# Kernel tuning notes

Measured on AMD Instinct MI355X. Metric: run time of the kernel, lower is better.

## Reference

```python
import jax, jax.numpy as jnp
import numpy as np
from jax import lax

B_, NCH, T = 128, 22, 1000
F1, F2 = 8, 16
BN_EPS = 1e-5


def _conv(x, w, b, pad, groups=1):
    y = lax.conv_general_dilated(x, w, (1, 1), pad,
                                 dimension_numbers=('NCHW', 'OIHW', 'NCHW'),
                                 feature_group_count=groups)
    return y if b is None else y + b[None, :, None, None]


def _bn(x, g, b):
    # eval-mode BatchNorm2d with running_mean=0, running_var=1
    return x * (g / np.sqrt(1.0 + BN_EPS))[None, :, None, None] + b[None, :, None, None]


def _avgpool(x, w, s):
    y = lax.reduce_window(x, 0.0, lax.add, (1, 1, 1, w), (1, 1, 1, s), 'VALID')
    return y / w


def _ln(x, g, b):
    m = x.mean(-1, keepdims=True)
    v = ((x - m) ** 2).mean(-1, keepdims=True)
    return (x - m) * lax.rsqrt(v + 1e-5) * g + b


def _enc_layer(h, qw, qb, pw, pb, f1w, f1b, f2w, f2b, g1, b1, g2, b2):
    # h: (S, N, E). Torch TransformerEncoderLayer default is seq-first, so axis 0
    # (the STDCNN batch dim) is attended over -- faithfully reproduced here.
    S, N, E = h.shape
    H = 8
    hd = E // H
    q, k, v = jnp.split(h @ qw.T + qb, 3, axis=-1)
    q = q.reshape(S, N, H, hd)
    k = k.reshape(S, N, H, hd)
    v = v.reshape(S, N, H, hd)
    att = jax.nn.softmax(jnp.einsum('snhd,tnhd->nhst', q, k) / np.sqrt(hd), axis=-1)
    o = jnp.einsum('nhst,tnhd->snhd', att, v).reshape(S, N, E) @ pw.T + pb
    h = _ln(h + o, g1, b1)
    ff = jax.nn.relu(h @ f1w.T + f1b) @ f2w.T + f2b
    return _ln(h + ff, g2, b2)


def setup_inputs() -> dict:
    key = jax.random.key(0)
    ks = iter(jax.random.split(key, 48))

    def nrm(shape, s=0.1):
        return jax.random.normal(next(ks), shape, jnp.float32) * s

    inp = dict(
        x=jax.random.normal(next(ks), (B_, 1, NCH, T), jnp.float32),
        w_spec1=nrm((F1, 1, 1, 125)), b_spec1=nrm((F1,)),
        w_spec2=nrm((F1, 1, 1, 30)), b_spec2=nrm((F1,)),
        g_bn1=1.0 + nrm((F1,)), b_bn1=nrm((F1,)),
        g_bn2=1.0 + nrm((F1,)), b_bn2=nrm((F1,)),
        w_sp1a=nrm((F2, 1, NCH, 1)),
        g_bn3=1.0 + nrm((F2,)), b_bn3=nrm((F2,)),
        w_sp1b=nrm((F2, F2, 1, 1)), b_sp1b=nrm((F2,)),
        g_bn4=1.0 + nrm((F2,)), b_bn4=nrm((F2,)),
        w_sp2=nrm((F2, F1, NCH, 1)), b_sp2=nrm((F2,)),
        g_bn5=1.0 + nrm((F2,)), b_bn5=nrm((F2,)),
        A=jnp.eye(F2, dtype=jnp.float32) + nrm((F2, F2), 0.01),
        Bm=nrm((F2, F2)),
        Cm=jnp.eye(F2, dtype=jnp.float32) + nrm((F2, F2), 0.01),
        qkv_w=nrm((2, 3 * F2, F2)), qkv_b=nrm((2, 3 * F2)),
        proj_w=nrm((2, F2, F2)), proj_b=nrm((2, F2)),
        ff1_w=nrm((2, 64, F2)), ff1_b=nrm((2, 64)),
        ff2_w=nrm((2, F2, 64)), ff2_b=nrm((2, F2)),
        ln1_g=jnp.ones((2, F2), jnp.float32), ln1_b=jnp.zeros((2, F2), jnp.float32),
        ln2_g=jnp.ones((2, F2), jnp.float32), ln2_b=jnp.zeros((2, F2), jnp.float32),
    )
    return inp


def reference(x, w_spec1, b_spec1, w_spec2, b_spec2, g_bn1, b_bn1, g_bn2, b_bn2,
              w_sp1a, g_bn3, b_bn3, w_sp1b, b_sp1b, g_bn4, b_bn4,
              w_sp2, b_sp2, g_bn5, b_bn5, A, Bm, Cm,
              qkv_w, qkv_b, proj_w, proj_b, ff1_w, ff1_b, ff2_w, ff2_b,
              ln1_g, ln1_b, ln2_g, ln2_b):
    # spectral branches (torch 'same' padding: k=125 -> (62,62); k=30 -> (14,15))
    x1 = _bn(_conv(x, w_spec1, b_spec1, [(0, 0), (62, 62)]), g_bn1, b_bn1)
    x2 = _bn(_conv(x, w_spec2, b_spec2, [(0, 0), (14, 15)]), g_bn2, b_bn2)
    # spatial branch 1 (dropout is identity in eval)
    s1 = jax.nn.elu(_bn(_conv(x1, w_sp1a, None, 'VALID', groups=F1), g_bn3, b_bn3))
    s1 = jax.nn.elu(_bn(_conv(s1, w_sp1b, b_sp1b, 'VALID'), g_bn4, b_bn4))
    s1 = _avgpool(s1, 32, 32)                                   # (B,16,1,31)
    # spatial branch 2: square -> avgpool -> log(clamp)
    s2 = _bn(_conv(x2, w_sp2, b_sp2, 'VALID'), g_bn5, b_bn5)
    s2 = jnp.log(jnp.clip(_avgpool(jnp.square(s2), 75, 25), 1e-6))  # (B,16,1,38)
    xc = jnp.concatenate([s1, s2], axis=3)                       # (B,16,1,69)
    Bn, Cc, H2, W2 = xc.shape
    seq = xc.reshape(Bn, Cc, H2 * W2).transpose(0, 2, 1)         # (B,L,16)

    # linear SSM recurrence (torch for-loop -> lax.scan)
    def step(state, xt):
        state = state @ A + xt @ Bm.T
        return state, state @ Cm.T

    _, outs = lax.scan(step, jnp.zeros((Bn, F2), seq.dtype), seq.transpose(1, 0, 2))
    h = outs.transpose(1, 0, 2)                                  # (B,L,16)

    for l in range(2):
        h = _enc_layer(h, qkv_w[l], qkv_b[l], proj_w[l], proj_b[l],
                       ff1_w[l], ff1_b[l], ff2_w[l], ff2_b[l],
                       ln1_g[l], ln1_b[l], ln2_g[l], ln2_b[l])

    return h.reshape(Bn, W2, 1, Cc).transpose(0, 3, 2, 1)        # (B,16,1,69)
```

## Files before the change

kernel.cpp:

```cpp
#include <hip/hip_runtime.h>
#include <hip/hip_bf16.h>
#include <math.h>

#define BBATCH 128
#define NCHAN  22
#define TLEN   1000
#define F1C    8
#define F2C    16
#define L1W    31
#define L2W    38
#define LSEQ   69
#define EDIM   16
#define NHEAD  8
#define FFDIM  64

#define C_SA   0
#define C_BA   16
#define C_BC2  32
#define C_W1P  3120
#define C_AW   (C_W1P + 1024)
#define C_TOTAL (C_AW + 5632)

#define OFF_CONST 0
#define OFF_CHNK  16384
#define OFF_SEQ   (OFF_CHNK + 81920)
#define OFF_STB   (OFF_SEQ + 141312)
#define OFF_HBUF  (OFF_STB + 141312)

typedef __attribute__((ext_vector_type(8))) short bf16x8;
typedef __attribute__((ext_vector_type(4))) float f32x4;

static __device__ __forceinline__ unsigned short f2bf(float f) {
    unsigned u = __float_as_uint(f);
    unsigned r = (u + 0x7FFFu + ((u >> 16) & 1u)) >> 16;
    return (unsigned short)r;
}

#define SWZ(v, imm) __int_as_float(__builtin_amdgcn_ds_swizzle(__float_as_int(v), imm))
#define MV16(dst, sv, W) do { \
    float p0=SWZ(sv,0x010)*W[0],  p1=SWZ(sv,0x030)*W[1],  \
          p2=SWZ(sv,0x050)*W[2],  p3=SWZ(sv,0x070)*W[3],  \
          p4=SWZ(sv,0x090)*W[4],  p5=SWZ(sv,0x0B0)*W[5],  \
          p6=SWZ(sv,0x0D0)*W[6],  p7=SWZ(sv,0x0F0)*W[7],  \
          p8=SWZ(sv,0x110)*W[8],  p9=SWZ(sv,0x130)*W[9],  \
          p10=SWZ(sv,0x150)*W[10],p11=SWZ(sv,0x170)*W[11],\
          p12=SWZ(sv,0x190)*W[12],p13=SWZ(sv,0x1B0)*W[13],\
          p14=SWZ(sv,0x1D0)*W[14],p15=SWZ(sv,0x1F0)*W[15];\
    dst = (((p0+p1)+(p2+p3))+((p4+p5)+(p6+p7))) + (((p8+p9)+(p10+p11))+((p12+p13)+(p14+p15))); \
} while(0)

__global__ void k_setup(const float* __restrict__ wsp1a, const float* __restrict__ b_spec1,
                        const float* __restrict__ g_bn1, const float* __restrict__ b_bn1,
                        const float* __restrict__ g_bn3, const float* __restrict__ b_bn3,
                        const float* __restrict__ w_spec2, const float* __restrict__ b_spec2,
                        const float* __restrict__ g_bn2, const float* __restrict__ b_bn2,
                        const float* __restrict__ w_sp2, const float* __restrict__ b_sp2,
                        const float* __restrict__ g_bn5, const float* __restrict__ b_bn5,
                        const float* __restrict__ w_spec1,
                        float* __restrict__ consts)
{
    int tid = threadIdx.x;
    int gb = blockIdx.x;
    int NG = gridDim.x;
    int gid = gb*256 + tid;
    float rbn = rsqrtf(1.0f + 1e-5f);
    if (gb == 0 && tid < 16) {
        int c2 = tid, c1 = c2 >> 1;
        float wsum = 0.f;
        for (int h = 0; h < NCHAN; h++) wsum += wsp1a[c2*NCHAN + h];
        float s1b = g_bn1[c1] * rbn;
        float s3  = g_bn3[c2] * rbn;
        float C1  = (s1b * b_spec1[c1] + b_bn1[c1]) * wsum;
        consts[C_SA + c2] = s3 * s1b;
        consts[C_BA + c2] = s3 * C1 + b_bn3[c2];
        float s5 = g_bn5[c2] * rbn;
        float acc = b_sp2[c2];
        for (int cc = 0; cc < F1C; cc++) {
            float s2b = g_bn2[cc] * rbn;
            float cb  = s2b * b_spec2[cc] + b_bn2[cc];
            float wsh = 0.f;
            for (int h = 0; h < NCHAN; h++) wsh += w_sp2[(c2*F1C + cc)*NCHAN + h];
            acc += wsh * cb;
        }
        consts[C_BC2 + c2] = s5 * acc + b_bn5[c2];
    }
    for (int idx = gid; idx < 8*128; idx += 256*NG) {
        int c1 = idx >> 7, k = idx & 127;
        consts[C_W1P + idx] = (k < 125) ? w_spec1[c1*125 + k] : 0.f;
    }
    unsigned* aw = (unsigned*)&consts[C_AW];
    for (int idx = gid; idx < 22*64*4; idx += 256*NG) {
        int r = idx & 3;
        int l = (idx >> 2) & 63;
        int c = idx >> 8;
        int m = l & 15;
        int k0 = ((l >> 4) << 3) + 2*r;
        float s5 = g_bn5[m] * rbn;
        float w0 = 0.f, w1 = 0.f;
        for (int cc = 0; cc < F1C; cc++) {
            float f = w_sp2[(m*F1C + cc)*NCHAN + c] * (g_bn2[cc] * rbn);
            if (k0 < 30)     w0 += f * w_spec2[cc*30 + k0];
            if (k0 + 1 < 30) w1 += f * w_spec2[cc*30 + k0 + 1];
        }
        w0 *= s5; w1 *= s5;
        aw[idx] = (unsigned)f2bf(w0) | ((unsigned)f2bf(w1) << 16);
    }
}

#define P1 260
#define P2 132
#define PW 132
#define PB2 288
#define SQP2 257
#define FRONT_SM 10448

__device__ __forceinline__ void b1f_body(float* smem, int bid,
    const float* __restrict__ x, const float* __restrict__ wsp1a,
    const float* __restrict__ consts,
    const float* __restrict__ w_sp1b, const float* __restrict__ b_sp1b,
    const float* __restrict__ g_bn4, const float* __restrict__ b_bn4,
    float* __restrict__ seq)
{
    float* mrow = smem;
    float* econv = smem + 16*P1;
    float* wlds = smem + 16*P1 + 16*P2;
    int q = bid & 7, b = bid >> 3;
    int tid = threadIdx.x;
    int t0 = q * 128;
    int NT = (q == 7) ? 104 : 128;
    int NCOL = NT + 124;

    for (int j = tid; j < NCOL; j += 256) {
        int t = t0 - 62 + j;
        float xv[NCHAN];
#pragma unroll
        for (int h = 0; h < NCHAN; h++)
            xv[h] = ((unsigned)t < 1000u) ? x[(b*NCHAN + h)*TLEN + t] : 0.f;
#pragma unroll
        for (int c2 = 0; c2 < 16; c2++) {
            float s = 0.f;
#pragma unroll
            for (int h = 0; h < NCHAN; h++) s += wsp1a[c2*NCHAN + h] * xv[h];
            mrow[c2*P1 + j] = s;
        }
    }
    for (int j = NCOL + tid; j < P1; j += 256) {
#pragma unroll
        for (int c2 = 0; c2 < 16; c2++) mrow[c2*P1 + j] = 0.f;
    }
    for (int i = tid; i < 1024; i += 256)
        wlds[(i >> 7)*PW + (i & 127)] = consts[C_W1P + i];
    __syncthreads();

    {
        int c2 = tid & 15, seg = tid >> 4, c1 = c2 >> 1;
        if (seg < ((NT + 7) >> 3)) {
            int u0 = seg * 8;
            const float* mr = &mrow[c2*P1 + u0];
            float sa = consts[C_SA + c2], ba = consts[C_BA + c2];
            float v[12];
            {
                float4 a0 = *(const float4*)&mr[0];
                float4 a1 = *(const float4*)&mr[4];
                float4 a2 = *(const float4*)&mr[8];
                v[0]=a0.x; v[1]=a0.y; v[2]=a0.z; v[3]=a0.w;
                v[4]=a1.x; v[5]=a1.y; v[6]=a1.z; v[7]=a1.w;
                v[8]=a2.x; v[9]=a2.y; v[10]=a2.z; v[11]=a2.w;
            }
            float acc[8];
#pragma unroll
            for (int u = 0; u < 8; u++) acc[u] = 0.f;
#pragma unroll
            for (int k0 = 0; k0 < 128; k0 += 4) {
                float w0 = wlds[c1*PW + k0 + 0];
                float w1 = wlds[c1*PW + k0 + 1];
                float w2 = wlds[c1*PW + k0 + 2];
                float w3 = wlds[c1*PW + k0 + 3];
#pragma unroll
                for (int u = 0; u < 8; u++) {
                    acc[u] += w0 * v[u+0];
                    acc[u] += w1 * v[u+1];
                    acc[u] += w2 * v[u+2];
                    acc[u] += w3 * v[u+3];
                }
                if (k0 < 124) {
#pragma unroll
                    for (int i = 0; i < 8; i++) v[i] = v[i+4];
                    float4 nv = *(const float4*)&mr[k0 + 12];
                    v[8]=nv.x; v[9]=nv.y; v[10]=nv.z; v[11]=nv.w;
                }
            }
            float e[8];
#pragma unroll
            for (int u = 0; u < 8; u++) {
                float a = sa * acc[u] + ba;
                e[u] = (a > 0.f) ? a : (expf(a) - 1.f);
            }
            float* ec = &econv[c2*P2 + u0];
            *(float4*)&ec[0] = make_float4(e[0], e[1], e[2], e[3]);
            *(float4*)&ec[4] = make_float4(e[4], e[5], e[6], e[7]);
        }
    }
    __syncthreads();

    if (tid < 128) {
        int u = tid;
        int w = 4*q + (u >> 5);
        float rbn = rsqrtf(1.0f + 1e-5f);
        float hv[16];
#pragma unroll
        for (int c = 0; c < 16; c++) hv[c] = econv[c*P2 + u];
        float p[16];
#pragma unroll
        for (int c = 0; c < 16; c++) {
            float s = 0.f;
#pragma unroll
            for (int j = 0; j < 16; j++) s += w_sp1b[c*16 + j] * hv[j];
            float sc = g_bn4[c] * rbn;
            float a = sc * (s + b_sp1b[c]) + b_bn4[c];
            float g = (a > 0.f) ? a : (expf(a) - 1.f);
            g += __shfl_xor(g, 1, 64);
            g += __shfl_xor(g, 2, 64);
            g += __shfl_xor(g, 4, 64);
            g += __shfl_xor(g, 8, 64);
            g += __shfl_xor(g, 16, 64);
            p[c] = g;
        }
        if ((u & 31) == 0 && w < L1W) {
            float* sp = &seq[(b*LSEQ + w)*16];
#pragma unroll
            for (int i = 0; i < 4; i++)
                *(float4*)&sp[4*i] = make_float4(p[4*i]*(1.f/32.f), p[4*i+1]*(1.f/32.f),
                                                 p[4*i+2]*(1.f/32.f), p[4*i+3]*(1.f/32.f));
        }
    }
}

__device__ __forceinline__ void b2mm_body(float* smem, int bid,
    const float* __restrict__ x, const float* __restrict__ consts,
    float* __restrict__ chnk)
{
    unsigned short* xs = (unsigned short*)smem;
    float* sq = smem + 6336;
    const unsigned* __restrict__ awg = (const unsigned*)&consts[C_AW];
    int q = bid & 3, b = bid >> 2;
    int t0 = q * 250;
    int tid = threadIdx.x;

    for (int idx = tid; idx < NCHAN*PB2; idx += 256) {
        int h = idx / PB2, e = idx - h*PB2;
        int t = t0 - 14 + e;
        const float* xr = x + (b*NCHAN + h)*TLEN;
        float v0 = ((unsigned)t < 1000u) ? xr[t] : 0.f;
        float v1 = ((unsigned)(t+1) < 1000u) ? xr[t+1] : 0.f;
        xs[idx] = f2bf(v0);
        xs[NCHAN*PB2 + idx] = f2bf(v1);
    }
    __syncthreads();

    int lane = tid & 63, wid = tid >> 6;
    int tp = lane & 15;
    int kb = (lane >> 4) << 3;
    int P = tp & 1;
    int tb0 = wid * 64;
    const unsigned short* xb = xs + P*(NCHAN*PB2) + (tb0 + tp + kb - P);

    f32x4 a0 = {0.f,0.f,0.f,0.f};
    f32x4 a1 = a0, a2 = a0, a3 = a0;
    for (int c = 0; c < NCHAN; c++) {
        bf16x8 af = *(const bf16x8*)(awg + (c*64 + lane)*4);
        const unsigned short* row = xb + c*PB2;
        union Uv { bf16x8 v; unsigned u[4]; };
        Uv B0, B1, B2, B3;
#pragma unroll
        for (int r = 0; r < 4; r++) {
            B0.u[r] = *(const unsigned*)(row + 2*r);
            B1.u[r] = *(const unsigned*)(row + 16 + 2*r);
            B2.u[r] = *(const unsigned*)(row + 32 + 2*r);
            B3.u[r] = *(const unsigned*)(row + 48 + 2*r);
        }
        a0 = __builtin_amdgcn_mfma_f32_16x16x32_bf16(af, B0.v, a0, 0, 0, 0);
        a1 = __builtin_amdgcn_mfma_f32_16x16x32_bf16(af, B1.v, a1, 0, 0, 0);
        a2 = __builtin_amdgcn_mfma_f32_16x16x32_bf16(af, B2.v, a2, 0, 0, 0);
        a3 = __builtin_amdgcn_mfma_f32_16x16x32_bf16(af, B3.v, a3, 0, 0, 0);
    }

    {
        int c2b = (lane >> 4) * 4;
        float bc[4];
#pragma unroll
        for (int r = 0; r < 4; r++) bc[r] = consts[C_BC2 + c2b + r];
#pragma unroll
        for (int r = 0; r < 4; r++) {
            float v;
            v = a0[r] + bc[r]; sq[(c2b+r)*SQP2 + tb0 + tp +  0] = v*v;
            v = a1[r] + bc[r]; sq[(c2b+r)*SQP2 + tb0 + tp + 16] = v*v;
            v = a2[r] + bc[r]; sq[(c2b+r)*SQP2 + tb0 + tp + 32] = v*v;
            v = a3[r] + bc[r]; sq[(c2b+r)*SQP2 + tb0 + tp + 48] = v*v;
        }
    }
    __syncthreads();

    if (tid < 160) {
        int c2 = tid / 10, ch = tid % 10;
        const float* s = &sq[c2*SQP2 + ch*25];
        float acc2 = 0.f;
#pragma unroll
        for (int i = 0; i < 25; i++) acc2 += s[i];
        chnk[(b*16 + c2)*40 + q*10 + ch] = acc2;
    }
}

__global__ __launch_bounds__(256, 2)
void k_front(const float* __restrict__ x, const float* __restrict__ wsp1a,
             const float* __restrict__ consts,
             const float* __restrict__ w_sp1b, const float* __restrict__ b_sp1b,
             const float* __restrict__ g_bn4, const float* __restrict__ b_bn4,
             float* __restrict__ seq, float* __restrict__ chnk)
{
    __shared__ __align__(16) float smem[FRONT_SM];
    int bid = blockIdx.x;
    if (bid < BBATCH*8) {
        b1f_body(smem, bid, x, wsp1a, consts, w_sp1b, b_sp1b, g_bn4, b_bn4, seq);
    } else {
        b2mm_body(smem, bid - BBATCH*8, x, consts, chnk);
    }
}

__global__ __launch_bounds__(64, 1)
void k_ssm(const float* __restrict__ seq, const float* __restrict__ chnk,
           const float* __restrict__ Amat, const float* __restrict__ Bmat,
           float* __restrict__ stbuf)
{
    int tid = threadIdx.x;
    int j = tid & 15;
    int b = blockIdx.x * 4 + (tid >> 4);

    float Acol[16], Brow[16];
#pragma unroll
    for (int i = 0; i < 16; i++) {
        Acol[i] = Amat[i*16 + j];
        Brow[i] = Bmat[j*16 + i];
    }

    float xv[LSEQ];
#pragma unroll
    for (int l = 0; l < 31; l++) xv[l] = seq[(b*LSEQ + l)*16 + j];
    {
        float cp[40];
        const float4* cpp = (const float4*)(chnk + (b*16 + j)*40);
#pragma unroll
        for (int i = 0; i < 10; i++) {
            float4 v = cpp[i];
            cp[4*i]=v.x; cp[4*i+1]=v.y; cp[4*i+2]=v.z; cp[4*i+3]=v.w;
        }
#pragma unroll
        for (int w = 0; w < 38; w++) {
            float m = (cp[w] + cp[w+1] + cp[w+2]) * (1.f/75.f);
            xv[31 + w] = logf(fmaxf(m, 1e-6f));
        }
    }

#pragma unroll
    for (int l = 0; l < LSEQ; l++) {
        float u;
        MV16(u, xv[l], Brow);
        xv[l] = u;
    }

    float st = 0.f;
#pragma unroll
    for (int l = 0; l < LSEQ; l++) {
        float nv;
        MV16(nv, st, Acol);
        st = nv + xv[l];
        stbuf[(l*BBATCH + b)*16 + j] = st;
    }
}

#define KVS2 38
__global__ __launch_bounds__(256, 2)
void k_tfl(const float* __restrict__ hin, const float* __restrict__ Cmat, int applyC,
           const float* __restrict__ qw, const float* __restrict__ qb,
           const float* __restrict__ pw, const float* __restrict__ pb,
           const float* __restrict__ f1w, const float* __restrict__ f1b,
           const float* __restrict__ f2w, const float* __restrict__ f2b,
           const float* __restrict__ g1, const float* __restrict__ b1,
           const float* __restrict__ g2, const float* __restrict__ b2,
           float* __restrict__ hout, float* __restrict__ fout, int writeFinal)
{
    __shared__ __align__(16) float sm[2176 + 128*KVS2 + 576 + 544 + 7*544 + 2048 + 64];
    float* h_l  = sm;
    float* kvq  = sm + 2176;
    float* qbuf = sm + 2176 + 128*KVS2;
    float* olds = qbuf + 576;
    float* ffp  = olds + 544;
    float* f1l  = ffp + 7*544;
    float* f2l  = f1l + 1024;
    float* f1bl = f2l + 1024;

    int tid = threadIdx.x;
    int rl = tid >> 3, hh = tid & 7;
    int n = blockIdx.x >> 2, q2 = blockIdx.x & 3;
    int s = q2*32 + rl;

    for (int i = tid; i < 1024; i += 256) { f1l[i] = f1w[i]; f2l[i] = f2w[i]; }
    if (tid < 64) f1bl[tid] = f1b[tid];

    {
        int r = tid >> 1, qd = tid & 1;
        if (applyC) {
            const float4* fr = (const float4*)(hin + (n*BBATCH + r)*16);
            float rv[16];
#pragma unroll
            for (int i = 0; i < 4; i++) {
                float4 a = fr[i];
                rv[4*i]=a.x; rv[4*i+1]=a.y; rv[4*i+2]=a.z; rv[4*i+3]=a.w;
            }
#pragma unroll
            for (int cq = 0; cq < 8; cq++) {
                int c = 8*qd + cq;
                float sum = 0.f;
#pragma unroll
                for (int i = 0; i < 16; i++) sum += rv[i] * Cmat[c*16 + i];
                h_l[r*17 + c] = sum;
            }
        } else {
            const float4* sr = (const float4*)(hin + (n*BBATCH + r)*16 + qd*8);
            float4 a0 = sr[0];
            float4 a1 = sr[1];
            h_l[r*17 + qd*8 + 0] = a0.x; h_l[r*17 + qd*8 + 1] = a0.y;
            h_l[r*17 + qd*8 + 2] = a0.z; h_l[r*17 + qd*8 + 3] = a0.w;
            h_l[r*17 + qd*8 + 4] = a1.x; h_l[r*17 + qd*8 + 5] = a1.y;
            h_l[r*17 + qd*8 + 6] = a1.z; h_l[r*17 + qd*8 + 7] = a1.w;
        }
    }
    __syncthreads();

    {
        int r2 = tid & 127;
        int ob = 16 + (tid >> 7) * 16;
        float hv[16];
#pragma unroll
        for (int c = 0; c < 16; c++) hv[c] = h_l[r2*17 + c];
#pragma unroll
        for (int oq = 0; oq < 16; oq++) {
            int o = ob + oq;
            float sum = qb[o];
#pragma unroll
            for (int c = 0; c < 16; c++) sum += qw[o*16 + c] * hv[c];
            kvq[r2*KVS2 + (o - 16)] = sum;
        }
        if (tid < 32) {
            int sr = q2*32 + tid;
            float hq[16];
#pragma unroll
            for (int c = 0; c < 16; c++) hq[c] = h_l[sr*17 + c];
#pragma unroll
            for (int o = 0; o < 16; o++) {
                float sum = qb[o];
#pragma unroll
                for (int c = 0; c < 16; c++) sum += qw[o*16 + c] * hq[c];
                qbuf[tid*18 + o] = sum;
            }
        }
    }
    __syncthreads();

    {
        const float SC = 1.0201941311775597f;
        float q0 = qbuf[rl*18 + 2*hh] * SC;
        float q1 = qbuf[rl*18 + 2*hh + 1] * SC;
        float m = -1e30f, su = 0.f, av = 0.f, bv = 0.f;
        for (int tb = 0; tb < 128; tb += 4) {
            float2 k0 = *(const float2*)&kvq[(tb+0)*KVS2 + 2*hh];
            float2 k1 = *(const float2*)&kvq[(tb+1)*KVS2 + 2*hh];
            float2 k2 = *(const float2*)&kvq[(tb+2)*KVS2 + 2*hh];
            float2 k3 = *(const float2*)&kvq[(tb+3)*KVS2 + 2*hh];
            float2 v0 = *(const float2*)&kvq[(tb+0)*KVS2 + 16 + 2*hh];
            float2 v1 = *(const float2*)&kvq[(tb+1)*KVS2 + 16 + 2*hh];
            float2 v2 = *(const float2*)&kvq[(tb+2)*KVS2 + 16 + 2*hh];
            float2 v3 = *(const float2*)&kvq[(tb+3)*KVS2 + 16 + 2*hh];
            float sc0 = q0*k0.x + q1*k0.y;
            float sc1 = q0*k1.x + q1*k1.y;
            float sc2 = q0*k2.x + q1*k2.y;
            float sc3 = q0*k3.x + q1*k3.y;
            float nm, c0, e;
            nm = fmaxf(m, sc0); c0 = exp2f(m - nm); e = exp2f(sc0 - nm);
            su = su*c0 + e; av = av*c0 + e*v0.x; bv = bv*c0 + e*v0.y; m = nm;
            nm = fmaxf(m, sc1); c0 = exp2f(m - nm); e = exp2f(sc1 - nm);
            su = su*c0 + e; av = av*c0 + e*v1.x; bv = bv*c0 + e*v1.y; m = nm;
            nm = fmaxf(m, sc2); c0 = exp2f(m - nm); e = exp2f(sc2 - nm);
            su = su*c0 + e; av = av*c0 + e*v2.x; bv = bv*c0 + e*v2.y; m = nm;
            nm = fmaxf(m, sc3); c0 = exp2f(m - nm); e = exp2f(sc3 - nm);
            su = su*c0 + e; av = av*c0 + e*v3.x; bv = bv*c0 + e*v3.y; m = nm;
        }
        float inv = 1.f / su;
        olds[rl*17 + 2*hh + 0] = av * inv;
        olds[rl*17 + 2*hh + 1] = bv * inv;
    }
    __syncthreads();

    {
        float rv[16], ov[16];
#pragma unroll
        for (int c = 0; c < 16; c++) { rv[c] = h_l[s*17 + c]; ov[c] = olds[rl*17 + c]; }
        float h1[16];
#pragma unroll
        for (int c = 0; c < 16; c++) {
            float p = pb[c];
#pragma unroll
            for (int j = 0; j < 16; j++) p += pw[c*16 + j] * ov[j];
            h1[c] = rv[c] + p;
        }
        float mn = 0.f;
#pragma unroll
        for (int c = 0; c < 16; c++) mn += h1[c];
        mn *= (1.f/16.f);
        float var = 0.f;
#pragma unroll
        for (int c = 0; c < 16; c++) { float d = h1[c] - mn; var += d*d; }
        var *= (1.f/16.f);
        float rs = rsqrtf(var + 1e-5f);
        float y[16];
#pragma unroll
        for (int c = 0; c < 16; c++) y[c] = (h1[c] - mn)*rs*g1[c] + b1[c];

        float t2[16];
#pragma unroll
        for (int c = 0; c < 16; c++) t2[c] = (hh == 0) ? f2b[c] : 0.f;
#pragma unroll
        for (int uq = 0; uq < 8; uq++) {
            int u = 8*hh + uq;
            float sv = f1bl[u];
#pragma unroll
            for (int c = 0; c < 16; c++) sv += f1l[u*16 + c] * y[c];
            sv = fmaxf(sv, 0.f);
#pragma unroll
            for (int c = 0; c < 16; c++) t2[c] += f2l[c*64 + u] * sv;
        }
        if (hh) {
#pragma unroll
            for (int c = 0; c < 16; c++) ffp[(hh-1)*544 + rl*17 + c] = t2[c];
        }
        __syncthreads();
        if (hh == 0) {
#pragma unroll
            for (int k = 0; k < 7; k++)
#pragma unroll
                for (int c = 0; c < 16; c++) t2[c] += ffp[k*544 + rl*17 + c];
            float h2[16];
#pragma unroll
            for (int c = 0; c < 16; c++) h2[c] = y[c] + t2[c];
            mn = 0.f;
#pragma unroll
            for (int c = 0; c < 16; c++) mn += h2[c];
            mn *= (1.f/16.f);
            var = 0.f;
#pragma unroll
            for (int c = 0; c < 16; c++) { float d = h2[c] - mn; var += d*d; }
            var *= (1.f/16.f);
            rs = rsqrtf(var + 1e-5f);
            if (writeFinal) {
#pragma unroll
                for (int c = 0; c < 16; c++)
                    fout[(s*16 + c)*LSEQ + n] = (h2[c] - mn)*rs*g2[c] + b2[c];
            } else {
                float z[16];
#pragma unroll
                for (int c = 0; c < 16; c++) z[c] = (h2[c] - mn)*rs*g2[c] + b2[c];
                float* hp = hout + (n*BBATCH + s)*16;
#pragma unroll
                for (int i = 0; i < 4; i++)
                    *(float4*)&hp[4*i] = make_float4(z[4*i], z[4*i+1], z[4*i+2], z[4*i+3]);
            }
        }
    }
}

extern "C" void kernel_launch(void* const* d_in, const int* in_sizes, int n_in,
                              void* d_out, int out_size, void* d_ws, size_t ws_size,
                              hipStream_t stream)
{
    const float* x       = (const float*)d_in[0];
    const float* w_spec1 = (const float*)d_in[1];
    const float* b_spec1 = (const float*)d_in[2];
    const float* w_spec2 = (const float*)d_in[3];
    const float* b_spec2 = (const float*)d_in[4];
    const float* g_bn1   = (const float*)d_in[5];
    const float* b_bn1   = (const float*)d_in[6];
    const float* g_bn2   = (const float*)d_in[7];
    const float* b_bn2   = (const float*)d_in[8];
    const float* w_sp1a  = (const float*)d_in[9];
    const float* g_bn3   = (const float*)d_in[10];
    const float* b_bn3   = (const float*)d_in[11];
    const float* w_sp1b  = (const float*)d_in[12];
    const float* b_sp1b  = (const float*)d_in[13];
    const float* g_bn4   = (const float*)d_in[14];
    const float* b_bn4   = (const float*)d_in[15];
    const float* w_sp2   = (const float*)d_in[16];
    const float* b_sp2   = (const float*)d_in[17];
    const float* g_bn5   = (const float*)d_in[18];
    const float* b_bn5   = (const float*)d_in[19];
    const float* Amat    = (const float*)d_in[20];
    const float* Bmat    = (const float*)d_in[21];
    const float* Cmat    = (const float*)d_in[22];
    const float* qkv_w   = (const float*)d_in[23];
    const float* qkv_b   = (const float*)d_in[24];
    const float* proj_w  = (const float*)d_in[25];
    const float* proj_b  = (const float*)d_in[26];
    const float* ff1_w   = (const float*)d_in[27];
    const float* ff1_b   = (const float*)d_in[28];
    const float* ff2_w   = (const float*)d_in[29];
    const float* ff2_b   = (const float*)d_in[30];
    const float* ln1_g   = (const float*)d_in[31];
    const float* ln1_b   = (const float*)d_in[32];
    const float* ln2_g   = (const float*)d_in[33];
    const float* ln2_b   = (const float*)d_in[34];

    float* ws  = (float*)d_ws;
    float* out = (float*)d_out;

    float* consts = ws + OFF_CONST;
    float* chnk   = ws + OFF_CHNK;
    float* seq    = ws + OFF_SEQ;
    float* stbuf  = ws + OFF_STB;
    float* hbuf   = ws + OFF_HBUF;

    k_setup<<<24, 256, 0, stream>>>(w_sp1a, b_spec1, g_bn1, b_bn1, g_bn3, b_bn3,
                                    w_spec2, b_spec2, g_bn2, b_bn2,
                                    w_sp2, b_sp2, g_bn5, b_bn5, w_spec1, consts);
    k_front<<<BBATCH*8 + BBATCH*4, 256, 0, stream>>>(x, w_sp1a, consts,
        w_sp1b, b_sp1b, g_bn4, b_bn4, seq, chnk);
    k_ssm<<<BBATCH/4, 64, 0, stream>>>(seq, chnk, Amat, Bmat, stbuf);

    k_tfl<<<LSEQ*4, 256, 0, stream>>>(stbuf, Cmat, 1,
        qkv_w, qkv_b, proj_w, proj_b, ff1_w, ff1_b, ff2_w, ff2_b,
        ln1_g, ln1_b, ln2_g, ln2_b, hbuf, out, 0);
    k_tfl<<<LSEQ*4, 256, 0, stream>>>(hbuf, Cmat, 0,
        qkv_w + 768, qkv_b + 48, proj_w + 256, proj_b + 16,
        ff1_w + 1024, ff1_b + 64, ff2_w + 1024, ff2_b + 16,
        ln1_g + 16, ln1_b + 16, ln2_g + 16, ln2_b + 16, hbuf, out, 1);
}
```

Before: 125.9 us.

## Compute spatial branch 1 front-end with bf16 MFMA using fused channel-temporal weights

Replaces the scalar FP32 path for branch 1 (channel mixing followed by a 125-tap temporal conv) with a single bf16 MFMA contraction over channels and taps. It uses combined per-channel, per-tap weights precomputed in the setup kernel, mirroring the existing branch-2 MFMA path. Each block now covers 256 time steps instead of 128, which halves the branch-1 block count. This cuts the large FP32 FMA count, but rounds inputs and weights to bf16 and enlarges the precomputed constants and workspace.

```diff
diff --git a/kernel.cpp b/kernel.cpp
--- a/kernel.cpp
+++ b/kernel.cpp
@@ -17,12 +17,12 @@
 #define C_SA   0
 #define C_BA   16
 #define C_BC2  32
-#define C_W1P  3120
-#define C_AW   (C_W1P + 1024)
-#define C_TOTAL (C_AW + 5632)
+#define C_AW   4144
+#define C_AW1  (C_AW + 5632)
+#define C_TOTAL (C_AW1 + 22528)
 
 #define OFF_CONST 0
-#define OFF_CHNK  16384
+#define OFF_CHNK  40960
 #define OFF_SEQ   (OFF_CHNK + 81920)
 #define OFF_STB   (OFF_SEQ + 141312)
 #define OFF_HBUF  (OFF_STB + 141312)
@@ -84,10 +84,6 @@
         }
         consts[C_BC2 + c2] = s5 * acc + b_bn5[c2];
     }
-    for (int idx = gid; idx < 8*128; idx += 256*NG) {
-        int c1 = idx >> 7, k = idx & 127;
-        consts[C_W1P + idx] = (k < 125) ? w_spec1[c1*125 + k] : 0.f;
-    }
     unsigned* aw = (unsigned*)&consts[C_AW];
     for (int idx = gid; idx < 22*64*4; idx += 256*NG) {
         int r = idx & 3;
@@ -105,111 +101,112 @@
         w0 *= s5; w1 *= s5;
         aw[idx] = (unsigned)f2bf(w0) | ((unsigned)f2bf(w1) << 16);
     }
-}
-
-#define P1 260
-#define P2 132
-#define PW 132
+    unsigned* aw1 = (unsigned*)&consts[C_AW1];
+    for (int idx = gid; idx < 22*4*64*4; idx += 256*NG) {
+        int r = idx & 3;
+        int l = (idx >> 2) & 63;
+        int kk = (idx >> 8) & 3;
+        int c = idx >> 10;
+        int m = l & 15;
+        int klocal = ((l >> 4) << 3) + 2*r;
+        int tap0 = kk*32 + klocal;
+        float sa = (g_bn3[m] * rbn) * (g_bn1[m >> 1] * rbn);
+        float base = sa * wsp1a[m*NCHAN + c];
+        float w0 = (tap0     < 125) ? base * w_spec1[(m >> 1)*125 + tap0]     : 0.f;
+        float w1 = (tap0 + 1 < 125) ? base * w_spec1[(m >> 1)*125 + tap0 + 1] : 0.f;
+        aw1[idx] = (unsigned)f2bf(w0) | ((unsigned)f2bf(w1) << 16);
+    }
+}
+
+#define PB1 384
+#define NW1 (NCHAN*PB1)
+#define PS1 257
 #define PB2 288
 #define SQP2 257
-#define FRONT_SM 10448
-
-__device__ __forceinline__ void b1f_body(float* smem, int bid,
-    const float* __restrict__ x, const float* __restrict__ wsp1a,
-    const float* __restrict__ consts,
+#define FRONT_SM 12560
+
+__device__ __forceinline__ void b1mm_body(float* smem, int bid,
+    const float* __restrict__ x, const float* __restrict__ consts,
     const float* __restrict__ w_sp1b, const float* __restrict__ b_sp1b,
     const float* __restrict__ g_bn4, const float* __restrict__ b_bn4,
     float* __restrict__ seq)
 {
-    float* mrow = smem;
-    float* econv = smem + 16*P1;
-    float* wlds = smem + 16*P1 + 16*P2;
-    int q = bid & 7, b = bid >> 3;
+    unsigned short* xs = (unsigned short*)smem;
+    float* sq = smem + 8448;
+    const uint4* __restrict__ awg = (const uint4*)&consts[C_AW1];
+    int q = bid & 3, b = bid >> 2;
+    int t0 = q * 256;
     int tid = threadIdx.x;
-    int t0 = q * 128;
-    int NT = (q == 7) ? 104 : 128;
-    int NCOL = NT + 124;
-
-    for (int j = tid; j < NCOL; j += 256) {
-        int t = t0 - 62 + j;
-        float xv[NCHAN];
-#pragma unroll
-        for (int h = 0; h < NCHAN; h++)
-            xv[h] = ((unsigned)t < 1000u) ? x[(b*NCHAN + h)*TLEN + t] : 0.f;
-#pragma unroll
-        for (int c2 = 0; c2 < 16; c2++) {
-            float s = 0.f;
-#pragma unroll
-            for (int h = 0; h < NCHAN; h++) s += wsp1a[c2*NCHAN + h] * xv[h];
-            mrow[c2*P1 + j] = s;
-        }
-    }
-    for (int j = NCOL + tid; j < P1; j += 256) {
-#pragma unroll
-        for (int c2 = 0; c2 < 16; c2++) mrow[c2*P1 + j] = 0.f;
-    }
-    for (int i = tid; i < 1024; i += 256)
-        wlds[(i >> 7)*PW + (i & 127)] = consts[C_W1P + i];
+
+    for (int idx = tid; idx < NW1; idx += 256) {
+        int h = idx / PB1, e = idx - h*PB1;
+        int t = t0 - 62 + e;
+        const float* xr = x + (b*NCHAN + h)*TLEN;
+        float v0 = ((unsigned)t < 1000u && e < 380) ? xr[t] : 0.f;
+        float v1 = ((unsigned)(t+1) < 1000u && e < 380) ? xr[t+1] : 0.f;
+        xs[idx] = f2bf(v0);
+        xs[NW1 + idx] = f2bf(v1);
+    }
     __syncthreads();
 
-    {
-        int c2 = tid & 15, seg = tid >> 4, c1 = c2 >> 1;
-        if (seg < ((NT + 7) >> 3)) {
-            int u0 = seg * 8;
-            const float* mr = &mrow[c2*P1 + u0];
-            float sa = consts[C_SA + c2], ba = consts[C_BA + c2];
-            float v[12];
-            {
-                float4 a0 = *(const float4*)&mr[0];
-                float4 a1 = *(const float4*)&mr[4];
-                float4 a2 = *(const float4*)&mr[8];
-                v[0]=a0.x; v[1]=a0.y; v[2]=a0.z; v[3]=a0.w;
-                v[4]=a1.x; v[5]=a1.y; v[6]=a1.z; v[7]=a1.w;
-                v[8]=a2.x; v[9]=a2.y; v[10]=a2.z; v[11]=a2.w;
+    int lane = tid & 63, wid = tid >> 6;
+    int tp = lane & 15;
+    int kb = (lane >> 4) << 3;
+    int P = tp & 1;
+    int tb0 = wid * 64;
+    const unsigned short* xb = xs + P*NW1 + (tb0 + tp + kb - P);
+
+    f32x4 a0 = {0.f,0.f,0.f,0.f};
+    f32x4 a1 = a0, a2 = a0, a3 = a0;
+    for (int c = 0; c < NCHAN; c++) {
+#pragma unroll
+        for (int kk = 0; kk < 4; kk++) {
+            uint4 au = awg[(c*4 + kk)*64 + lane];
+            union Ua { uint4 q; bf16x8 v; } A; A.q = au;
+            const unsigned short* row = xb + c*PB1 + kk*32;
+            union Uv { bf16x8 v; unsigned u[4]; };
+            Uv B0, B1, B2, B3;
+#pragma unroll
+            for (int r = 0; r < 4; r++) {
+                B0.u[r] = *(const unsigned*)(row + 2*r);
+                B1.u[r] = *(const unsigned*)(row + 16 + 2*r);
+                B2.u[r] = *(const unsigned*)(row + 32 + 2*r);
+                B3.u[r] = *(const unsigned*)(row + 48 + 2*r);
             }
-            float acc[8];
-#pragma unroll
-            for (int u = 0; u < 8; u++) acc[u] = 0.f;
-#pragma unroll
-            for (int k0 = 0; k0 < 128; k0 += 4) {
-                float w0 = wlds[c1*PW + k0 + 0];
-                float w1 = wlds[c1*PW + k0 + 1];
-                float w2 = wlds[c1*PW + k0 + 2];
-                float w3 = wlds[c1*PW + k0 + 3];
-#pragma unroll
-                for (int u = 0; u < 8; u++) {
-                    acc[u] += w0 * v[u+0];
-                    acc[u] += w1 * v[u+1];
-                    acc[u] += w2 * v[u+2];
-                    acc[u] += w3 * v[u+3];
-                }
-                if (k0 < 124) {
-#pragma unroll
-                    for (int i = 0; i < 8; i++) v[i] = v[i+4];
-                    float4 nv = *(const float4*)&mr[k0 + 12];
-                    v[8]=nv.x; v[9]=nv.y; v[10]=nv.z; v[11]=nv.w;
-                }
-            }
-            float e[8];
-#pragma unroll
-            for (int u = 0; u < 8; u++) {
-                float a = sa * acc[u] + ba;
-                e[u] = (a > 0.f) ? a : (expf(a) - 1.f);
-            }
-            float* ec = &econv[c2*P2 + u0];
-            *(float4*)&ec[0] = make_float4(e[0], e[1], e[2], e[3]);
-            *(float4*)&ec[4] = make_float4(e[4], e[5], e[6], e[7]);
+            a0 = __builtin_amdgcn_mfma_f32_16x16x32_bf16(A.v, B0.v, a0, 0, 0, 0);
+            a1 = __builtin_amdgcn_mfma_f32_16x16x32_bf16(A.v, B1.v, a1, 0, 0, 0);
+            a2 = __builtin_amdgcn_mfma_f32_16x16x32_bf16(A.v, B2.v, a2, 0, 0, 0);
+            a3 = __builtin_amdgcn_mfma_f32_16x16x32_bf16(A.v, B3.v, a3, 0, 0, 0);
+        }
+    }
+
+    {
+        int c2b = (lane >> 4) * 4;
+        float ba[4];
+#pragma unroll
+        for (int r = 0; r < 4; r++) ba[r] = consts[C_BA + c2b + r];
+#pragma unroll
+        for (int r = 0; r < 4; r++) {
+            float v, e;
+            v = a0[r] + ba[r]; e = (v > 0.f) ? v : (expf(v) - 1.f);
+            sq[(c2b+r)*PS1 + tb0 + tp +  0] = e;
+            v = a1[r] + ba[r]; e = (v > 0.f) ? v : (expf(v) - 1.f);
+            sq[(c2b+r)*PS1 + tb0 + tp + 16] = e;
+            v = a2[r] + ba[r]; e = (v > 0.f) ? v : (expf(v) - 1.f);
+            sq[(c2b+r)*PS1 + tb0 + tp + 32] = e;
+            v = a3[r] + ba[r]; e = (v > 0.f) ? v : (expf(v) - 1.f);
+            sq[(c2b+r)*PS1 + tb0 + tp + 48] = e;
         }
     }
     __syncthreads();
 
-    if (tid < 128) {
+    {
         int u = tid;
-        int w = 4*q + (u >> 5);
+        int w = 8*q + (u >> 5);
         float rbn = rsqrtf(1.0f + 1e-5f);
         float hv[16];
 #pragma unroll
-        for (int c = 0; c < 16; c++) hv[c] = econv[c*P2 + u];
+        for (int c = 0; c < 16; c++) hv[c] = sq[c*PS1 + u];
         float p[16];
 #pragma unroll
         for (int c = 0; c < 16; c++) {
@@ -312,7 +309,7 @@
 }
 
 __global__ __launch_bounds__(256, 2)
-void k_front(const float* __restrict__ x, const float* __restrict__ wsp1a,
+void k_front(const float* __restrict__ x,
              const float* __restrict__ consts,
              const float* __restrict__ w_sp1b, const float* __restrict__ b_sp1b,
              const float* __restrict__ g_bn4, const float* __restrict__ b_bn4,
@@ -320,10 +317,10 @@
 {
     __shared__ __align__(16) float smem[FRONT_SM];
     int bid = blockIdx.x;
-    if (bid < BBATCH*8) {
-        b1f_body(smem, bid, x, wsp1a, consts, w_sp1b, b_sp1b, g_bn4, b_bn4, seq);
+    if (bid < BBATCH*4) {
+        b1mm_body(smem, bid, x, consts, w_sp1b, b_sp1b, g_bn4, b_bn4, seq);
     } else {
-        b2mm_body(smem, bid - BBATCH*8, x, consts, chnk);
+        b2mm_body(smem, bid - BBATCH*4, x, consts, chnk);
     }
 }
 
@@ -630,7 +627,7 @@
     k_setup<<<24, 256, 0, stream>>>(w_sp1a, b_spec1, g_bn1, b_bn1, g_bn3, b_bn3,
                                     w_spec2, b_spec2, g_bn2, b_bn2,
                                     w_sp2, b_sp2, g_bn5, b_bn5, w_spec1, consts);
-    k_front<<<BBATCH*8 + BBATCH*4, 256, 0, stream>>>(x, w_sp1a, consts,
+    k_front<<<BBATCH*4 + BBATCH*4, 256, 0, stream>>>(x, consts,
         w_sp1b, b_sp1b, g_bn4, b_bn4, seq, chnk);
     k_ssm<<<BBATCH/4, 64, 0, stream>>>(seq, chnk, Amat, Bmat, stbuf);
 
```

Result: faster. 121.9 us (-3.1%).
